# Kernel optimization log

Measured on AMD Instinct MI355X. Metric: run time of the kernel, lower is better.

The kernel has to match this reference:

```python
import jax, jax.numpy as jnp
import numpy as np

NEG_SLOPE = 0.2  # PyG GATConv default


def _gat_conv(x, src, dst, W, a_src, a_dst, bias, concat):
    # x: [N, F_in]; W: [H*C, F_in]; a_src/a_dst: [H, C]; src/dst: [E]
    n = x.shape[0]
    H, C = a_src.shape
    h = (x @ W.T).reshape(n, H, C)                       # [N, H, C]
    al_src = (h * a_src[None]).sum(-1)                   # [N, H]
    al_dst = (h * a_dst[None]).sum(-1)                   # [N, H]
    e = jax.nn.leaky_relu(al_src[src] + al_dst[dst], NEG_SLOPE)  # [E, H]
    # scatter-softmax over incoming edges of each dst node
    m = jax.ops.segment_max(e, dst, num_segments=n)      # [N, H]
    e = jnp.exp(e - m[dst])
    denom = jax.ops.segment_sum(e, dst, num_segments=n)  # [N, H]
    alpha = e / denom[dst]                               # [E, H]
    out = jax.ops.segment_sum(alpha[:, :, None] * h[src], dst, num_segments=n)  # [N, H, C]
    if concat:
        out = out.reshape(n, H * C)
    else:
        out = out.mean(axis=1)
    return out + bias


def setup_inputs() -> dict:
    key = jax.random.key(0)
    ks = jax.random.split(key, 16)
    N, E = 20000, 640000
    IN, HID, HEADS, OUT, HLSTM, NCLS = 256, 32, 4, 64, 32, 1
    s = 0.1
    return {
        "x": jax.random.normal(ks[0], (N, IN), jnp.float32),
        "conv1_w": jax.random.normal(ks[1], (HID * HEADS, IN), jnp.float32) * s,
        "conv1_att_src": jax.random.normal(ks[2], (HEADS, HID), jnp.float32) * s,
        "conv1_att_dst": jax.random.normal(ks[3], (HEADS, HID), jnp.float32) * s,
        "conv1_bias": jnp.zeros((HID * HEADS,), jnp.float32),
        "conv2_w": jax.random.normal(ks[4], (OUT, HID * HEADS), jnp.float32) * s,
        "conv2_att_src": jax.random.normal(ks[5], (1, OUT), jnp.float32) * s,
        "conv2_att_dst": jax.random.normal(ks[6], (1, OUT), jnp.float32) * s,
        "conv2_bias": jnp.zeros((OUT,), jnp.float32),
        "lstm_w_ih": jax.random.normal(ks[7], (4 * HLSTM, OUT), jnp.float32) * s,
        "lstm_w_hh": jax.random.normal(ks[8], (4 * HLSTM, HLSTM), jnp.float32) * s,
        "lstm_b_ih": jnp.zeros((4 * HLSTM,), jnp.float32),
        "lstm_b_hh": jnp.zeros((4 * HLSTM,), jnp.float32),
        "fc_w": jax.random.normal(ks[9], (NCLS, HLSTM), jnp.float32) * s,
        "fc_b": jnp.zeros((NCLS,), jnp.float32),
        "edge_index": jax.random.randint(ks[10], (2, E), 0, N, jnp.int64),
    }


def reference(x, conv1_w, conv1_att_src, conv1_att_dst, conv1_bias,
              conv2_w, conv2_att_src, conv2_att_dst, conv2_bias,
              lstm_w_ih, lstm_w_hh, lstm_b_ih, lstm_b_hh,
              fc_w, fc_b, edge_index):
    N = x.shape[0]
    loops = jnp.arange(N, dtype=edge_index.dtype)  # add_self_loops=True (PyG default)
    src = jnp.concatenate([edge_index[0], loops])
    dst = jnp.concatenate([edge_index[1], loops])

    h = _gat_conv(x, src, dst, conv1_w, conv1_att_src, conv1_att_dst, conv1_bias, concat=True)
    h = jax.nn.elu(h)
    h = _gat_conv(h, src, dst, conv2_w, conv2_att_src, conv2_att_dst, conv2_bias, concat=False)

    # LSTM over the node sequence, batch=1 (x.view(-1, N, out_dim))
    Hs = lstm_w_hh.shape[1]
    pre = h @ lstm_w_ih.T + (lstm_b_ih + lstm_b_hh)      # [N, 4H] input projections

    def step(carry, p):
        hp, cp = carry
        g = p + hp @ lstm_w_hh.T
        i, f, gg, o = jnp.split(g, 4)
        c = jax.nn.sigmoid(f) * cp + jax.nn.sigmoid(i) * jnp.tanh(gg)
        hn = jax.nn.sigmoid(o) * jnp.tanh(c)
        return (hn, c), hn

    init = (jnp.zeros((Hs,), x.dtype), jnp.zeros((Hs,), x.dtype))
    _, seq = jax.lax.scan(step, init, pre)               # [N, H]
    out = seq @ fc_w.T + fc_b                            # [N, num_classes]
    return out[None]                                     # [1, N, num_classes]
```

## Files before the change

kernel.cpp:

```cpp
#include <hip/hip_runtime.h>
#include <hip/hip_bf16.h>
#include <hip/hip_fp16.h>
#include <cstdint>
#include <cstddef>

#define LOG2E 1.44269504088896340736f
#define SLOTW 128
#define SCAP 32

typedef float v2f __attribute__((ext_vector_type(2)));
typedef _Float16 f16x8 __attribute__((ext_vector_type(8)));
typedef float f32x4 __attribute__((ext_vector_type(4)));

template<int M, int K, bool BIAS, bool AL, int H, bool HOUT, bool SCAT>
__global__ __launch_bounds__(256)
void gemm_mfma(const float* __restrict__ A, const float* __restrict__ B,
               const float* __restrict__ bias0, const float* __restrict__ bias1,
               const float* __restrict__ asrc, const float* __restrict__ adst,
               float* __restrict__ als, float* __restrict__ ald,
               float* __restrict__ C, __half* __restrict__ Ch, int N,
               const int* __restrict__ esrc, const int* __restrict__ edst,
               int* __restrict__ cnt, unsigned short* __restrict__ slots,
               int E, int gemmBlocks) {
  if constexpr (SCAT) {
    if ((int)blockIdx.x >= gemmBlocks) {
      int base = ((int)blockIdx.x - gemmBlocks) * 1024 + (int)threadIdx.x * 4;
      if (base + 3 < E) {
        int4 ss = *(const int4*)(esrc + base);
        int4 dd = *(const int4*)(edst + base);
        int p0 = atomicAdd(&cnt[dd.x], 1);
        int p1 = atomicAdd(&cnt[N + dd.y], 1);
        int p2 = atomicAdd(&cnt[2 * N + dd.z], 1);
        int p3 = atomicAdd(&cnt[3 * N + dd.w], 1);
        if (p0 < SCAP) slots[(size_t)dd.x * SLOTW + p0] = (unsigned short)ss.x;
        if (p1 < SCAP) slots[(size_t)dd.y * SLOTW + 32 + p1] = (unsigned short)ss.y;
        if (p2 < SCAP) slots[(size_t)dd.z * SLOTW + 64 + p2] = (unsigned short)ss.z;
        if (p3 < SCAP) slots[(size_t)dd.w * SLOTW + 96 + p3] = (unsigned short)ss.w;
      } else if (base < E) {
        for (int t = base; t < E; ++t) {
          int s = esrc[t], d = edst[t];
          int j = t & 3;
          int pos = atomicAdd(&cnt[j * N + d], 1);
          if (pos < SCAP) slots[(size_t)d * SLOTW + j * 32 + pos] = (unsigned short)s;
        }
      }
      return;
    }
  }
  constexpr int TN = 64, KB = 32;
  constexpr int LDH = 40;
  constexpr int WCOL = (M >= 128) ? 2 : 1;
  constexpr int WROW = 4 / WCOL;
  constexpr int RT = TN / WROW;
  constexpr int CTW = M / WCOL;
  constexpr int RF = RT / 16;
  constexpr int CF = CTW / 16;

  __shared__ __align__(16) _Float16 As[TN * LDH];
  __shared__ __align__(16) _Float16 Bs[M * LDH];

  const int tid = threadIdx.x;
  const int n0 = blockIdx.x * TN;
  const int w = tid >> 6, lane = tid & 63;
  const int wr = w / WCOL, wc = w % WCOL;
  const int lr = lane & 15, lg = lane >> 4;

  f32x4 acc[RF][CF];
#pragma unroll
  for (int rf = 0; rf < RF; ++rf)
#pragma unroll
    for (int cf = 0; cf < CF; ++cf) acc[rf][cf] = (f32x4){0.f, 0.f, 0.f, 0.f};

  const int arow = tid >> 2, akq = (tid & 3) * 8;
  const int bcol = tid >> 1, bkq = (tid & 1) * 16;

  for (int k0 = 0; k0 < K; k0 += KB) {
    {
      int gn = n0 + arow;
      float4 v0 = make_float4(0.f, 0.f, 0.f, 0.f), v1 = v0;
      if (gn < N) {
        const float* ap = A + (size_t)gn * K + k0 + akq;
        v0 = *(const float4*)ap;
        v1 = *(const float4*)(ap + 4);
      }
      f16x8 h;
      h[0] = (_Float16)v0.x; h[1] = (_Float16)v0.y; h[2] = (_Float16)v0.z; h[3] = (_Float16)v0.w;
      h[4] = (_Float16)v1.x; h[5] = (_Float16)v1.y; h[6] = (_Float16)v1.z; h[7] = (_Float16)v1.w;
      *(f16x8*)&As[arow * LDH + akq] = h;
    }
    if (bcol < M) {
      const float* bp = B + (size_t)bcol * K + k0 + bkq;
      float4 v0 = *(const float4*)bp;
      float4 v1 = *(const float4*)(bp + 4);
      float4 v2 = *(const float4*)(bp + 8);
      float4 v3 = *(const float4*)(bp + 12);
      f16x8 h0, h1;
      h0[0] = (_Float16)v0.x; h0[1] = (_Float16)v0.y; h0[2] = (_Float16)v0.z; h0[3] = (_Float16)v0.w;
      h0[4] = (_Float16)v1.x; h0[5] = (_Float16)v1.y; h0[6] = (_Float16)v1.z; h0[7] = (_Float16)v1.w;
      h1[0] = (_Float16)v2.x; h1[1] = (_Float16)v2.y; h1[2] = (_Float16)v2.z; h1[3] = (_Float16)v2.w;
      h1[4] = (_Float16)v3.x; h1[5] = (_Float16)v3.y; h1[6] = (_Float16)v3.z; h1[7] = (_Float16)v3.w;
      *(f16x8*)&Bs[bcol * LDH + bkq] = h0;
      *(f16x8*)&Bs[bcol * LDH + bkq + 8] = h1;
    }
    __syncthreads();
    f16x8 af[RF], bf[CF];
#pragma unroll
    for (int rf = 0; rf < RF; ++rf)
      af[rf] = *(const f16x8*)&As[(wr * RT + rf * 16 + lr) * LDH + 8 * lg];
#pragma unroll
    for (int cf = 0; cf < CF; ++cf)
      bf[cf] = *(const f16x8*)&Bs[(wc * CTW + cf * 16 + lr) * LDH + 8 * lg];
#pragma unroll
    for (int rf = 0; rf < RF; ++rf)
#pragma unroll
      for (int cf = 0; cf < CF; ++cf)
        acc[rf][cf] = __builtin_amdgcn_mfma_f32_16x16x32_f16(af[rf], bf[cf], acc[rf][cf], 0, 0, 0);
    __syncthreads();
  }

  const int colbase = wc * CTW;
  float bv[CF];
#pragma unroll
  for (int cf = 0; cf < CF; ++cf) {
    if constexpr (BIAS) bv[cf] = bias0[colbase + cf * 16 + lr] + bias1[colbase + cf * 16 + lr];
    else bv[cf] = 0.f;
  }
#pragma unroll
  for (int rf = 0; rf < RF; ++rf) {
#pragma unroll
    for (int reg = 0; reg < 4; ++reg) {
      const int gr = n0 + wr * RT + rf * 16 + lg * 4 + reg;
      if (gr < N) {
#pragma unroll
        for (int cf = 0; cf < CF; ++cf) {
          float v = acc[rf][cf][reg] + bv[cf];
          if constexpr (HOUT) Ch[(size_t)gr * M + colbase + cf * 16 + lr] = __float2half(v);
          else                C[(size_t)gr * M + colbase + cf * 16 + lr] = v;
        }
      }
    }
  }
  if constexpr (AL) {
    constexpr int CPH = M / H;
    constexpr int FPH = CPH / 16;
    constexpr int HPW = CTW / CPH;
    float as_v[CF], ad_v[CF];
#pragma unroll
    for (int cf = 0; cf < CF; ++cf) {
      as_v[cf] = asrc[colbase + cf * 16 + lr];
      ad_v[cf] = adst[colbase + cf * 16 + lr];
    }
#pragma unroll
    for (int rf = 0; rf < RF; ++rf) {
#pragma unroll
      for (int reg = 0; reg < 4; ++reg) {
        const int gr = n0 + wr * RT + rf * 16 + lg * 4 + reg;
#pragma unroll
        for (int hh = 0; hh < HPW; ++hh) {
          float ps = 0.f, pd = 0.f;
#pragma unroll
          for (int f = 0; f < FPH; ++f) {
            const int cf = hh * FPH + f;
            ps = fmaf(acc[rf][cf][reg], as_v[cf], ps);
            pd = fmaf(acc[rf][cf][reg], ad_v[cf], pd);
          }
#pragma unroll
          for (int m = 1; m < 16; m <<= 1) { ps += __shfl_xor(ps, m); pd += __shfl_xor(pd, m); }
          if (lr == 0 && gr < N) {
            const int head = (colbase + hh * CPH) / CPH;
            als[(size_t)gr * H + head] = ps;
            ald[(size_t)gr * H + head] = pd;
          }
        }
      }
    }
  }
}

template<int M, int K, bool BIAS>
__global__ __launch_bounds__(256)
void gemm_nt(const float* __restrict__ A, const float* __restrict__ B,
             const float* __restrict__ bias0, const float* __restrict__ bias1,
             float* __restrict__ C, int N) {
  constexpr int TN = 64, KB = 32;
  constexpr int CT = M / 4;
  constexpr int NR = (TN * M) / 1024;
  constexpr int WT = (M * KB) / 1024;
  __shared__ __align__(16) float xs[KB][TN + 4];
  __shared__ __align__(16) float ws[KB][M + 4];
  const int tid = threadIdx.x;
  const int tc = tid % CT, tr = tid / CT;
  const int n0 = blockIdx.x * TN;
  float acc[NR][4];
#pragma unroll
  for (int r = 0; r < NR; ++r) { acc[r][0] = acc[r][1] = acc[r][2] = acc[r][3] = 0.f; }

  for (int k0 = 0; k0 < K; k0 += KB) {
#pragma unroll
    for (int u = 0; u < 2; ++u) {
      int slot = u * 256 + tid;
      int node = slot >> 3, kv = (slot & 7) * 4;
      int gn = n0 + node;
      float4 v = make_float4(0.f, 0.f, 0.f, 0.f);
      if (gn < N) v = *(const float4*)(A + (size_t)gn * K + k0 + kv);
      xs[kv + 0][node] = v.x; xs[kv + 1][node] = v.y; xs[kv + 2][node] = v.z; xs[kv + 3][node] = v.w;
    }
#pragma unroll
    for (int u = 0; u < WT; ++u) {
      int slot = u * 256 + tid;
      int col = slot >> 3, kv = (slot & 7) * 4;
      float4 v = *(const float4*)(B + (size_t)col * K + k0 + kv);
      ws[kv + 0][col] = v.x; ws[kv + 1][col] = v.y; ws[kv + 2][col] = v.z; ws[kv + 3][col] = v.w;
    }
    __syncthreads();
#pragma unroll
    for (int kk = 0; kk < KB; ++kk) {
      float4 wv = *(const float4*)&ws[kk][tc * 4];
      float4 va = *(const float4*)&xs[kk][tr * NR];
      float4 vb = va;
      if constexpr (NR == 8) vb = *(const float4*)&xs[kk][tr * NR + 4];
      float xr[NR];
      xr[0] = va.x; xr[1] = va.y; xr[2] = va.z; xr[3] = va.w;
      if constexpr (NR == 8) { xr[4] = vb.x; xr[5] = vb.y; xr[6] = vb.z; xr[7] = vb.w; }
#pragma unroll
      for (int r = 0; r < NR; ++r) {
        acc[r][0] = fmaf(xr[r], wv.x, acc[r][0]);
        acc[r][1] = fmaf(xr[r], wv.y, acc[r][1]);
        acc[r][2] = fmaf(xr[r], wv.z, acc[r][2]);
        acc[r][3] = fmaf(xr[r], wv.w, acc[r][3]);
      }
    }
    __syncthreads();
  }
  float b[4] = {0.f, 0.f, 0.f, 0.f};
  if constexpr (BIAS) {
#pragma unroll
    for (int c = 0; c < 4; ++c) b[c] = bias0[tc * 4 + c] + bias1[tc * 4 + c];
  }
#pragma unroll
  for (int r = 0; r < NR; ++r) {
    int gn = n0 + tr * NR + r;
    if (gn < N) {
      float4 o = make_float4(acc[r][0] + b[0], acc[r][1] + b[1], acc[r][2] + b[2], acc[r][3] + b[3]);
      *(float4*)(C + (size_t)gn * M + tc * 4) = o;
    }
  }
}

template<int D, int H, bool ELU, int CAP>
__global__ __launch_bounds__(D)
void conv_edge(const __half* __restrict__ hsrc, const float* __restrict__ als,
               const float* __restrict__ ald, const float* __restrict__ bias,
               const int* __restrict__ cnt, const unsigned short* __restrict__ slots,
               const int* __restrict__ esrc, const int* __restrict__ edst, int E,
               float* __restrict__ out, int N) {
  constexpr int C = D / H;
  const int n = blockIdx.x;
  const int tid = threadIdx.x;
  const int myh = tid / C;
  const int c0 = cnt[n], c1 = cnt[N + n], c2 = cnt[2 * N + n], c3 = cnt[3 * N + n];
  const int deg_r = c0 + c1 + c2 + c3;
  const int deg = deg_r + 1;
  const bool ok = (c0 <= SCAP) && (c1 <= SCAP) && (c2 <= SCAP) && (c3 <= SCAP) && (deg <= CAP);

  __shared__ __align__(16) float lw[CAP][H];
  __shared__ int sidx[CAP];
  __shared__ float red[2][H];

  float ad[H];
#pragma unroll
  for (int hh = 0; hh < H; ++hh) ad[hh] = ald[(size_t)n * H + hh];

  float acc = 0.f;
  float myinv;
  if (ok) {
    const int b0 = c0, b1 = c0 + c1, b2 = b1 + c2;
    float sm[H];
#pragma unroll
    for (int hh = 0; hh < H; ++hh) sm[hh] = 0.f;
    const unsigned short* srow = slots + (size_t)n * SLOTW;
    for (int e = tid; e < deg; e += D) {
      int s;
      if (e == 0) s = n;
      else {
        int idx = e - 1, off;
        if (idx < b0)      off = idx;
        else if (idx < b1) off = 32 + (idx - b0);
        else if (idx < b2) off = 64 + (idx - b1);
        else               off = 96 + (idx - b2);
        s = (int)srow[off];
      }
      sidx[e] = s * (D * 2);
      if constexpr (H == 4) {
        float4 a4 = *(const float4*)(als + (size_t)s * 4);
        float l0 = a4.x + ad[0]; l0 = l0 > 0.f ? l0 : 0.2f * l0;
        float l1 = a4.y + ad[1]; l1 = l1 > 0.f ? l1 : 0.2f * l1;
        float l2 = a4.z + ad[2]; l2 = l2 > 0.f ? l2 : 0.2f * l2;
        float l3 = a4.w + ad[3]; l3 = l3 > 0.f ? l3 : 0.2f * l3;
        float w0 = __builtin_amdgcn_exp2f(LOG2E * l0);
        float w1 = __builtin_amdgcn_exp2f(LOG2E * l1);
        float w2 = __builtin_amdgcn_exp2f(LOG2E * l2);
        float w3 = __builtin_amdgcn_exp2f(LOG2E * l3);
        *(float4*)&lw[e][0] = make_float4(w0, w1, w2, w3);
        sm[0] += w0; sm[1] += w1; sm[2] += w2; sm[3] += w3;
      } else {
        float x = als[s] + ad[0];
        x = x > 0.f ? x : 0.2f * x;
        float w = __builtin_amdgcn_exp2f(LOG2E * x);
        lw[e][0] = w;
        sm[0] += w;
      }
    }
#pragma unroll
    for (int hh = 0; hh < H; ++hh) {
#pragma unroll
      for (int m = 32; m >= 1; m >>= 1) sm[hh] += __shfl_xor(sm[hh], m);
    }
    if constexpr (D > 64) {
      if ((tid & 63) == 0) {
#pragma unroll
        for (int hh = 0; hh < H; ++hh) red[tid >> 6][hh] = sm[hh];
      }
      __syncthreads();
#pragma unroll
      for (int hh = 0; hh < H; ++hh) sm[hh] = red[0][hh] + red[1][hh];
    }
    myinv = 1.0f / sm[myh];
    __syncthreads();
    const char* hb = (const char*)hsrc + (size_t)tid * 2;
#pragma unroll 8
    for (int e = 0; e < deg; ++e) {
      float w = lw[e][myh];
      int ofs = sidx[e];
      float hv = __half2float(*(const __half*)(hb + ofs));
      acc = fmaf(w, hv, acc);
    }
  } else {
    float mx[H];
#pragma unroll
    for (int hh = 0; hh < H; ++hh) {
      float xs_ = als[(size_t)n * H + hh] + ad[hh];
      xs_ = xs_ > 0.f ? xs_ : 0.2f * xs_;
      mx[hh] = xs_;
    }
    for (int e = tid; e < E; e += D) {
      if (edst[e] != n) continue;
      int s = esrc[e];
#pragma unroll
      for (int hh = 0; hh < H; ++hh) {
        float x = als[(size_t)s * H + hh] + ad[hh];
        x = x > 0.f ? x : 0.2f * x;
        mx[hh] = fmaxf(mx[hh], x);
      }
    }
#pragma unroll
    for (int hh = 0; hh < H; ++hh) {
#pragma unroll
      for (int m = 32; m >= 1; m >>= 1) mx[hh] = fmaxf(mx[hh], __shfl_xor(mx[hh], m));
    }
    if constexpr (D > 64) {
      if ((tid & 63) == 0) {
#pragma unroll
        for (int hh = 0; hh < H; ++hh) red[tid >> 6][hh] = mx[hh];
      }
      __syncthreads();
#pragma unroll
      for (int hh = 0; hh < H; ++hh) mx[hh] = fmaxf(red[0][hh], red[1][hh]);
      __syncthreads();
    }
    float sm[H];
#pragma unroll
    for (int hh = 0; hh < H; ++hh) sm[hh] = 0.f;
    if (tid == 0) {
#pragma unroll
      for (int hh = 0; hh < H; ++hh) {
        float x = als[(size_t)n * H + hh] + ad[hh];
        x = x > 0.f ? x : 0.2f * x;
        sm[hh] += __builtin_amdgcn_exp2f(LOG2E * (x - mx[hh]));
      }
    }
    for (int e = tid; e < E; e += D) {
      if (edst[e] != n) continue;
      int s = esrc[e];
#pragma unroll
      for (int hh = 0; hh < H; ++hh) {
        float x = als[(size_t)s * H + hh] + ad[hh];
        x = x > 0.f ? x : 0.2f * x;
        sm[hh] += __builtin_amdgcn_exp2f(LOG2E * (x - mx[hh]));
      }
    }
#pragma unroll
    for (int hh = 0; hh < H; ++hh) {
#pragma unroll
      for (int m = 32; m >= 1; m >>= 1) sm[hh] += __shfl_xor(sm[hh], m);
    }
    if constexpr (D > 64) {
      if ((tid & 63) == 0) {
#pragma unroll
        for (int hh = 0; hh < H; ++hh) red[tid >> 6][hh] = sm[hh];
      }
      __syncthreads();
#pragma unroll
      for (int hh = 0; hh < H; ++hh) sm[hh] = red[0][hh] + red[1][hh];
    }
    const float myad = ad[myh], mym = mx[myh];
    myinv = 1.0f / sm[myh];
    {
      float x = als[(size_t)n * H + myh] + myad;
      x = x > 0.f ? x : 0.2f * x;
      float w = __builtin_amdgcn_exp2f(LOG2E * (x - mym));
      acc = fmaf(w, __half2float(hsrc[(size_t)n * D + tid]), acc);
    }
    for (int e = 0; e < E; ++e) {
      if (edst[e] != n) continue;
      int s = esrc[e];
      float x = als[(size_t)s * H + myh] + myad;
      x = x > 0.f ? x : 0.2f * x;
      float w = __builtin_amdgcn_exp2f(LOG2E * (x - mym));
      acc = fmaf(w, __half2float(hsrc[(size_t)s * D + tid]), acc);
    }
  }
  float v = fmaf(acc, myinv, bias[tid]);
  if constexpr (ELU) v = v > 0.f ? v : (__builtin_amdgcn_exp2f(LOG2E * v) - 1.0f);
  out[(size_t)n * D + tid] = v;
}

#define LSTM_S 24
#define LSTM_W 64
__global__ __attribute__((amdgpu_waves_per_eu(1, 1))) __launch_bounds__(64)
void lstm_kernel(const float* __restrict__ pre, const float* __restrict__ whh,
                 const float* __restrict__ fcw, const float* __restrict__ fcb,
                 float* __restrict__ out, int N) {
  constexpr int U = 8;
  const int lane = threadIdx.x;
  const int k = lane & 31, half = lane >> 5;
  const int row0 = k + 32 * half;
  const int row1 = 64 + k + 32 * half;

  const int t0 = blockIdx.x * LSTM_S;
  const int tb = max(0, t0 - LSTM_W);
  const int te = min(t0 + LSTM_S, N);

  v2f wp[32];
#pragma unroll
  for (int j = 0; j < 32; ++j) {
    wp[j].x = whh[row0 * 32 + j];
    wp[j].y = whh[row1 * 32 + j];
  }
  const float mult_y = half ? -LOG2E : 2.0f * LOG2E;
  const float m1 = half ? 1.0f : -2.0f;
  const float a1c = half ? 0.0f : 1.0f;
  const float myfw = fcw[k];
  const float fcb0 = fcb[0];

  float hn = 0.f, cp = 0.f;
  float c0[U], c1[U], n0[U], n1[U];
  const float* pb = pre + (size_t)tb * 128;
#pragma unroll
  for (int u = 0; u < U; ++u) {
    c0[u] = pb[(size_t)u * 128 + row0];
    c1[u] = pb[(size_t)u * 128 + row1];
  }
#pragma unroll
  for (int u = 0; u < U; ++u) {
    n0[u] = pb[(size_t)(U + u) * 128 + row0];
    n1[u] = pb[(size_t)(U + u) * 128 + row1];
  }

#pragma unroll 1
  for (int t = tb; t < te; t += U) {
#pragma unroll
    for (int u = 0; u < U; ++u) {
      v2f acc0 = {c0[u], c1[u]};
      v2f acc1 = {0.f, 0.f}, acc2 = {0.f, 0.f}, acc3 = {0.f, 0.f};
      const int hni = __float_as_int(hn);
#pragma unroll
      for (int j = 0; j < 8; ++j) {
        float s = __int_as_float(__builtin_amdgcn_readlane(hni, 32 + j));
        v2f ss = {s, s};
        acc0 = __builtin_elementwise_fma(ss, wp[j], acc0);
      }
#pragma unroll
      for (int j = 8; j < 16; ++j) {
        float s = __int_as_float(__builtin_amdgcn_readlane(hni, 32 + j));
        v2f ss = {s, s};
        acc1 = __builtin_elementwise_fma(ss, wp[j], acc1);
      }
#pragma unroll
      for (int j = 16; j < 24; ++j) {
        float s = __int_as_float(__builtin_amdgcn_readlane(hni, 32 + j));
        v2f ss = {s, s};
        acc2 = __builtin_elementwise_fma(ss, wp[j], acc2);
      }
#pragma unroll
      for (int j = 24; j < 32; ++j) {
        float s = __int_as_float(__builtin_amdgcn_readlane(hni, 32 + j));
        v2f ss = {s, s};
        acc3 = __builtin_elementwise_fma(ss, wp[j], acc3);
      }
      v2f a01 = (acc0 + acc1) + (acc2 + acc3);
      float ax = a01.x;
      float ay = a01.y;
      float e0 = __builtin_amdgcn_exp2f(-LOG2E * ax);
      float sa = __builtin_amdgcn_rcpf(1.0f + e0);
      float e1 = __builtin_amdgcn_exp2f(mult_y * ay);
      float r1 = __builtin_amdgcn_rcpf(1.0f + e1);
      float v1 = fmaf(r1, m1, a1c);
      float op2 = half ? cp : v1;
      float q = sa * op2;
      float xu = __shfl_xor(q, 32, 64);
      float c = q + xu;
      cp = c;
      float e2 = __builtin_amdgcn_exp2f(2.0f * LOG2E * c);
      float r2 = __builtin_amdgcn_rcpf(1.0f + e2);
      float tc = fmaf(r2, -2.0f, 1.0f);
      hn = v1 * tc;
      const int tt = t + u;
      if (tt >= t0) {
        float p = hn * myfw;
        p += __shfl_xor(p, 16); p += __shfl_xor(p, 8); p += __shfl_xor(p, 4);
        p += __shfl_xor(p, 2);  p += __shfl_xor(p, 1);
        if (lane == 32) out[tt] = p + fcb0;
      }
    }
#pragma unroll
    for (int u = 0; u < U; ++u) { c0[u] = n0[u]; c1[u] = n1[u]; }
    const float* nx = pre + (size_t)(t + 2 * U) * 128;
#pragma unroll
    for (int u = 0; u < U; ++u) {
      n0[u] = nx[(size_t)u * 128 + row0];
      n1[u] = nx[(size_t)u * 128 + row1];
    }
  }
}

extern "C" void kernel_launch(void* const* d_in, const int* in_sizes, int n_in,
                              void* d_out, int out_size, void* d_ws, size_t ws_size,
                              hipStream_t stream) {
  const float* x   = (const float*)d_in[0];
  const float* w1  = (const float*)d_in[1];
  const float* a1s = (const float*)d_in[2];
  const float* a1d = (const float*)d_in[3];
  const float* b1  = (const float*)d_in[4];
  const float* w2  = (const float*)d_in[5];
  const float* a2s = (const float*)d_in[6];
  const float* a2d = (const float*)d_in[7];
  const float* b2  = (const float*)d_in[8];
  const float* wih = (const float*)d_in[9];
  const float* whh = (const float*)d_in[10];
  const float* bih = (const float*)d_in[11];
  const float* bhh = (const float*)d_in[12];
  const float* fcw = (const float*)d_in[13];
  const float* fcb = (const float*)d_in[14];
  const int*   ei  = (const int*)d_in[15];
  const int N = in_sizes[0] / 256;
  const int E = in_sizes[15] / 2;
  const int* esrc = ei;
  const int* edst = ei + E;

  float* fw = (float*)d_ws;
  size_t o = 0;
  __half* h1h = (__half*)(fw + o); o += (size_t)N * 64;
  __half* h2h = (__half*)(fw + o); o += (size_t)N * 32;
  float* x2   = fw + o; o += (size_t)N * 128;
  float* h3   = fw + o; o += (size_t)N * 64;
  float* pre  = fw + o; o += (size_t)(N + 16) * 128;
  float* al1s = fw + o; o += (size_t)N * 4;
  float* al1d = fw + o; o += (size_t)N * 4;
  float* al2s = fw + o; o += (size_t)N;
  float* al2d = fw + o; o += (size_t)N;
  int* cnt = (int*)(fw + o); o += (size_t)4 * N;
  unsigned short* slots = (unsigned short*)(fw + o);

  const int eb = (E + 1023) / 1024;
  const int gb = (N + 63) / 64;
  const int lstm_blocks = (N + LSTM_S - 1) / LSTM_S;

  hipMemsetAsync(cnt, 0, (size_t)4 * N * sizeof(int), stream);

  hipLaunchKernelGGL((gemm_mfma<128, 256, false, true, 4, true, true>),
                     dim3(gb + eb), dim3(256), 0, stream,
                     x, w1, (const float*)nullptr, (const float*)nullptr,
                     a1s, a1d, al1s, al1d, (float*)nullptr, h1h, N,
                     esrc, edst, cnt, slots, E, gb);

  hipLaunchKernelGGL((conv_edge<128, 4, true, 160>), dim3(N), dim3(128), 0, stream,
                     h1h, al1s, al1d, b1, cnt, slots, esrc, edst, E, x2, N);

  hipLaunchKernelGGL((gemm_mfma<64, 128, false, true, 1, true, false>),
                     dim3(gb), dim3(256), 0, stream,
                     x2, w2, (const float*)nullptr, (const float*)nullptr,
                     a2s, a2d, al2s, al2d, (float*)nullptr, h2h, N,
                     (const int*)nullptr, (const int*)nullptr, (int*)nullptr,
                     (unsigned short*)nullptr, 0, 0);
  hipLaunchKernelGGL((conv_edge<64, 1, false, 160>), dim3(N), dim3(64), 0, stream,
                     h2h, al2s, al2d, b2, cnt, slots, esrc, edst, E, h3, N);

  hipLaunchKernelGGL((gemm_nt<128, 64, true>),
                     dim3(gb), dim3(256), 0, stream,
                     h3, wih, bih, bhh, pre, N);
  hipLaunchKernelGGL(lstm_kernel, dim3(lstm_blocks), dim3(64), 0, stream,
                     pre, whh, fcw, fcb, (float*)d_out, N);
}
```

Before: 230.4 us.

## Add specialized first-layer MFMA GEMM with smaller row tiles and register prefetch

Replaces the generic templated GEMM for the first GAT projection with a dedicated kernel that uses 32-row tiles, a K-block of 64, and register double-buffering of the global loads for the next K step. Each wave owns one head's 32 columns, which makes the attention-logit reduction a simple 16-lane shuffle per head. The edge-scatter part moves into the new kernel, and the generic template drops its scatter path. The aim is more blocks for occupancy and load latency hidden behind MFMA work, at the cost of reloading the 128x256 weight matrix twice as many times.

```diff
diff --git a/kernel.cpp b/kernel.cpp
--- a/kernel.cpp
+++ b/kernel.cpp
@@ -11,6 +11,162 @@
 typedef float v2f __attribute__((ext_vector_type(2)));
 typedef _Float16 f16x8 __attribute__((ext_vector_type(8)));
 typedef float f32x4 __attribute__((ext_vector_type(4)));
+
+__global__ __launch_bounds__(256, 2)
+void gemm1_mfma(const float* __restrict__ A, const float* __restrict__ B,
+                const float* __restrict__ asrc, const float* __restrict__ adst,
+                float* __restrict__ als, float* __restrict__ ald,
+                __half* __restrict__ Ch, int N,
+                const int* __restrict__ esrc, const int* __restrict__ edst,
+                int* __restrict__ cnt, unsigned short* __restrict__ slots,
+                int E, int gemmBlocks) {
+  if ((int)blockIdx.x >= gemmBlocks) {
+    int base = ((int)blockIdx.x - gemmBlocks) * 1024 + (int)threadIdx.x * 4;
+    if (base + 3 < E) {
+      int4 ss = *(const int4*)(esrc + base);
+      int4 dd = *(const int4*)(edst + base);
+      int p0 = atomicAdd(&cnt[dd.x], 1);
+      int p1 = atomicAdd(&cnt[N + dd.y], 1);
+      int p2 = atomicAdd(&cnt[2 * N + dd.z], 1);
+      int p3 = atomicAdd(&cnt[3 * N + dd.w], 1);
+      if (p0 < SCAP) slots[(size_t)dd.x * SLOTW + p0] = (unsigned short)ss.x;
+      if (p1 < SCAP) slots[(size_t)dd.y * SLOTW + 32 + p1] = (unsigned short)ss.y;
+      if (p2 < SCAP) slots[(size_t)dd.z * SLOTW + 64 + p2] = (unsigned short)ss.z;
+      if (p3 < SCAP) slots[(size_t)dd.w * SLOTW + 96 + p3] = (unsigned short)ss.w;
+    } else if (base < E) {
+      for (int t = base; t < E; ++t) {
+        int s = esrc[t], d = edst[t];
+        int j = t & 3;
+        int pos = atomicAdd(&cnt[j * N + d], 1);
+        if (pos < SCAP) slots[(size_t)d * SLOTW + j * 32 + pos] = (unsigned short)s;
+      }
+    }
+    return;
+  }
+  constexpr int M = 128, K = 256, TN = 32, KB = 64;
+  constexpr int LDH = 72;
+  constexpr int RF = 2, CF = 2;
+  constexpr int NS = K / KB;
+
+  __shared__ __align__(16) _Float16 As[TN * LDH];
+  __shared__ __align__(16) _Float16 Bs[M * LDH];
+
+  const int tid = threadIdx.x;
+  const int n0 = blockIdx.x * TN;
+  const int w = tid >> 6, lane = tid & 63;
+  const int lr = lane & 15, lg = lane >> 4;
+  const int colbase = w * 32;
+
+  const int ar = tid >> 3;
+  const int ak = (tid & 7) * 8;
+  const int gnA = n0 + ar;
+
+  f32x4 acc[RF][CF];
+#pragma unroll
+  for (int rf = 0; rf < RF; ++rf)
+#pragma unroll
+    for (int cf = 0; cf < CF; ++cf) acc[rf][cf] = (f32x4){0.f, 0.f, 0.f, 0.f};
+
+  float4 pa0, pa1;
+  float4 pb[8];
+
+  const float* aRow = A + (size_t)gnA * K + ak;
+
+#define LOADG(k0)                                                              \
+  do {                                                                         \
+    if (gnA < N) { pa0 = *(const float4*)(aRow + (k0));                        \
+                   pa1 = *(const float4*)(aRow + (k0) + 4); }                  \
+    else { pa0 = make_float4(0.f,0.f,0.f,0.f); pa1 = pa0; }                    \
+    _Pragma("unroll")                                                          \
+    for (int c = 0; c < 4; ++c) {                                              \
+      int cid = c * 256 + tid;                                                 \
+      int brow = cid >> 3, bk = (cid & 7) * 8;                                 \
+      const float* bp = B + (size_t)brow * K + (k0) + bk;                      \
+      pb[2*c]   = *(const float4*)bp;                                          \
+      pb[2*c+1] = *(const float4*)(bp + 4);                                    \
+    }                                                                          \
+  } while (0)
+
+  LOADG(0);
+  for (int s = 0; s < NS; ++s) {
+    {
+      f16x8 h;
+      h[0]=(_Float16)pa0.x; h[1]=(_Float16)pa0.y; h[2]=(_Float16)pa0.z; h[3]=(_Float16)pa0.w;
+      h[4]=(_Float16)pa1.x; h[5]=(_Float16)pa1.y; h[6]=(_Float16)pa1.z; h[7]=(_Float16)pa1.w;
+      *(f16x8*)&As[ar * LDH + ak] = h;
+#pragma unroll
+      for (int c = 0; c < 4; ++c) {
+        int cid = c * 256 + tid;
+        int brow = cid >> 3, bk = (cid & 7) * 8;
+        f16x8 hb;
+        hb[0]=(_Float16)pb[2*c].x; hb[1]=(_Float16)pb[2*c].y;
+        hb[2]=(_Float16)pb[2*c].z; hb[3]=(_Float16)pb[2*c].w;
+        hb[4]=(_Float16)pb[2*c+1].x; hb[5]=(_Float16)pb[2*c+1].y;
+        hb[6]=(_Float16)pb[2*c+1].z; hb[7]=(_Float16)pb[2*c+1].w;
+        *(f16x8*)&Bs[brow * LDH + bk] = hb;
+      }
+    }
+    __syncthreads();
+    if (s + 1 < NS) LOADG((s + 1) * KB);
+    {
+      f16x8 af[2][RF], bf[2][CF];
+#pragma unroll
+      for (int ks = 0; ks < 2; ++ks) {
+#pragma unroll
+        for (int rf = 0; rf < RF; ++rf)
+          af[ks][rf] = *(const f16x8*)&As[(rf * 16 + lr) * LDH + ks * 32 + 8 * lg];
+#pragma unroll
+        for (int cf = 0; cf < CF; ++cf)
+          bf[ks][cf] = *(const f16x8*)&Bs[(colbase + cf * 16 + lr) * LDH + ks * 32 + 8 * lg];
+      }
+#pragma unroll
+      for (int ks = 0; ks < 2; ++ks)
+#pragma unroll
+        for (int rf = 0; rf < RF; ++rf)
+#pragma unroll
+          for (int cf = 0; cf < CF; ++cf)
+            acc[rf][cf] = __builtin_amdgcn_mfma_f32_16x16x32_f16(af[ks][rf], bf[ks][cf], acc[rf][cf], 0, 0, 0);
+    }
+    __syncthreads();
+  }
+#undef LOADG
+
+#pragma unroll
+  for (int rf = 0; rf < RF; ++rf) {
+#pragma unroll
+    for (int reg = 0; reg < 4; ++reg) {
+      const int gr = n0 + rf * 16 + lg * 4 + reg;
+      if (gr < N) {
+#pragma unroll
+        for (int cf = 0; cf < CF; ++cf)
+          Ch[(size_t)gr * M + colbase + cf * 16 + lr] = __float2half(acc[rf][cf][reg]);
+      }
+    }
+  }
+  {
+    float as_v[CF], ad_v[CF];
+#pragma unroll
+    for (int cf = 0; cf < CF; ++cf) {
+      as_v[cf] = asrc[colbase + cf * 16 + lr];
+      ad_v[cf] = adst[colbase + cf * 16 + lr];
+    }
+#pragma unroll
+    for (int rf = 0; rf < RF; ++rf) {
+#pragma unroll
+      for (int reg = 0; reg < 4; ++reg) {
+        const int gr = n0 + rf * 16 + lg * 4 + reg;
+        float ps = acc[rf][0][reg] * as_v[0] + acc[rf][1][reg] * as_v[1];
+        float pd = acc[rf][0][reg] * ad_v[0] + acc[rf][1][reg] * ad_v[1];
+#pragma unroll
+        for (int m = 1; m < 16; m <<= 1) { ps += __shfl_xor(ps, m); pd += __shfl_xor(pd, m); }
+        if (lr == 0 && gr < N) {
+          als[(size_t)gr * 4 + w] = ps;
+          ald[(size_t)gr * 4 + w] = pd;
+        }
+      }
+    }
+  }
+}
 
 template<int M, int K, bool BIAS, bool AL, int H, bool HOUT, bool SCAT>
 __global__ __launch_bounds__(256)
@@ -22,31 +178,6 @@
                const int* __restrict__ esrc, const int* __restrict__ edst,
                int* __restrict__ cnt, unsigned short* __restrict__ slots,
                int E, int gemmBlocks) {
-  if constexpr (SCAT) {
-    if ((int)blockIdx.x >= gemmBlocks) {
-      int base = ((int)blockIdx.x - gemmBlocks) * 1024 + (int)threadIdx.x * 4;
-      if (base + 3 < E) {
-        int4 ss = *(const int4*)(esrc + base);
-        int4 dd = *(const int4*)(edst + base);
-        int p0 = atomicAdd(&cnt[dd.x], 1);
-        int p1 = atomicAdd(&cnt[N + dd.y], 1);
-        int p2 = atomicAdd(&cnt[2 * N + dd.z], 1);
-        int p3 = atomicAdd(&cnt[3 * N + dd.w], 1);
-        if (p0 < SCAP) slots[(size_t)dd.x * SLOTW + p0] = (unsigned short)ss.x;
-        if (p1 < SCAP) slots[(size_t)dd.y * SLOTW + 32 + p1] = (unsigned short)ss.y;
-        if (p2 < SCAP) slots[(size_t)dd.z * SLOTW + 64 + p2] = (unsigned short)ss.z;
-        if (p3 < SCAP) slots[(size_t)dd.w * SLOTW + 96 + p3] = (unsigned short)ss.w;
-      } else if (base < E) {
-        for (int t = base; t < E; ++t) {
-          int s = esrc[t], d = edst[t];
-          int j = t & 3;
-          int pos = atomicAdd(&cnt[j * N + d], 1);
-          if (pos < SCAP) slots[(size_t)d * SLOTW + j * 32 + pos] = (unsigned short)s;
-        }
-      }
-      return;
-    }
-  }
   constexpr int TN = 64, KB = 32;
   constexpr int LDH = 40;
   constexpr int WCOL = (M >= 128) ? 2 : 1;
@@ -573,16 +704,15 @@
   unsigned short* slots = (unsigned short*)(fw + o);
 
   const int eb = (E + 1023) / 1024;
+  const int gb1 = (N + 31) / 32;
   const int gb = (N + 63) / 64;
   const int lstm_blocks = (N + LSTM_S - 1) / LSTM_S;
 
   hipMemsetAsync(cnt, 0, (size_t)4 * N * sizeof(int), stream);
 
-  hipLaunchKernelGGL((gemm_mfma<128, 256, false, true, 4, true, true>),
-                     dim3(gb + eb), dim3(256), 0, stream,
-                     x, w1, (const float*)nullptr, (const float*)nullptr,
-                     a1s, a1d, al1s, al1d, (float*)nullptr, h1h, N,
-                     esrc, edst, cnt, slots, E, gb);
+  hipLaunchKernelGGL(gemm1_mfma, dim3(gb1 + eb), dim3(256), 0, stream,
+                     x, w1, a1s, a1d, al1s, al1d, h1h, N,
+                     esrc, edst, cnt, slots, E, gb1);
 
   hipLaunchKernelGGL((conv_edge<128, 4, true, 160>), dim3(N), dim3(128), 0, stream,
                      h1h, al1s, al1d, b1, cnt, slots, esrc, edst, E, x2, N);
```

After: 227.7 us. No clear change (-1.2%).
